# Kernel optimization log

Measured on AMD Instinct MI355X. Metric: run time of the kernel, lower is better.

The kernel has to match this reference:

```python
import jax, jax.numpy as jnp
import numpy as np

V = 32000   # vocab
T = 256     # context len
C = 384     # n_embed
H = 6       # heads
D = 64      # head dim (HEAD_SIZE // NUM_HEADS)
L = 6       # blocks
B = 16      # batch
FF = 4 * C


def setup_inputs() -> dict:
    key = jax.random.key(0)
    ks = jax.random.split(key, 16)
    s = 0.02
    p = {}
    p["x_ids"] = jax.random.randint(ks[0], (B, T), 0, V)
    p["y_ids"] = jax.random.randint(ks[1], (B, T), 0, V)
    p["tok_emb"] = jax.random.normal(ks[2], (V, C), jnp.float32) * s
    p["pos_emb"] = jax.random.normal(ks[3], (T, C), jnp.float32) * s
    p["Wq"] = jax.random.normal(ks[4], (L, H, C, D), jnp.float32) * s
    p["Wk"] = jax.random.normal(ks[5], (L, H, C, D), jnp.float32) * s
    p["Wv"] = jax.random.normal(ks[6], (L, H, C, D), jnp.float32) * s
    p["Wo"] = jax.random.normal(ks[7], (L, H * D, C), jnp.float32) * s
    p["bo"] = jnp.zeros((L, C), jnp.float32)
    p["ln1_s"] = jnp.ones((L, C), jnp.float32)
    p["ln1_b"] = jnp.zeros((L, C), jnp.float32)
    p["ln2_s"] = jnp.ones((L, C), jnp.float32)
    p["ln2_b"] = jnp.zeros((L, C), jnp.float32)
    p["W1"] = jax.random.normal(ks[8], (L, C, FF), jnp.float32) * s
    p["b1"] = jnp.zeros((L, FF), jnp.float32)
    p["W2"] = jax.random.normal(ks[9], (L, FF, C), jnp.float32) * s
    p["b2"] = jnp.zeros((L, C), jnp.float32)
    p["lnf_s"] = jnp.ones((C,), jnp.float32)
    p["lnf_b"] = jnp.zeros((C,), jnp.float32)
    p["Whead"] = jax.random.normal(ks[10], (C, V), jnp.float32) * s
    p["bhead"] = jnp.zeros((V,), jnp.float32)
    return p


def _ln(x, scale, bias, eps=1e-5):
    m = x.mean(-1, keepdims=True)
    v = ((x - m) ** 2).mean(-1, keepdims=True)
    return (x - m) * jax.lax.rsqrt(v + eps) * scale + bias


def reference(x_ids, y_ids, tok_emb, pos_emb, Wq, Wk, Wv, Wo, bo,
              ln1_s, ln1_b, ln2_s, ln2_b, W1, b1, W2, b2,
              lnf_s, lnf_b, Whead, bhead):
    Bq, Tq = x_ids.shape
    x = tok_emb[x_ids] + pos_emb[:Tq]                      # [B,T,C]
    mask = jnp.tril(jnp.ones((Tq, Tq), bool))
    scale = C ** -0.5  # NOTE: original scales by input dim C, not head dim
    for l in range(L):
        h = _ln(x, ln1_s[l], ln1_b[l])
        q = jnp.einsum('btc,hcd->bhtd', h, Wq[l])
        k = jnp.einsum('btc,hcd->bhtd', h, Wk[l])
        v = jnp.einsum('btc,hcd->bhtd', h, Wv[l])
        att = jnp.einsum('bhtd,bhsd->bhts', q, k) * scale
        att = jnp.where(mask, att, -jnp.inf)
        att = jax.nn.softmax(att, axis=-1)
        o = jnp.einsum('bhts,bhsd->bhtd', att, v)
        o = o.transpose(0, 2, 1, 3).reshape(Bq, Tq, H * D)  # concat heads
        x = x + o @ Wo[l] + bo[l]
        h2 = _ln(x, ln2_s[l], ln2_b[l])
        x = x + jax.nn.relu(h2 @ W1[l] + b1[l]) @ W2[l] + b2[l]
    x = _ln(x, lnf_s, lnf_b)
    logits = x @ Whead + bhead                             # [B,T,V]
    logp = jax.nn.log_softmax(logits, axis=-1)
    loss = -jnp.take_along_axis(logp, y_ids[..., None], axis=-1).mean()
    return (logits, loss)
```

## Files before the change

kernel.cpp:

```cpp
#include <hip/hip_runtime.h>

typedef unsigned short u16;
typedef u16   u16x4 __attribute__((ext_vector_type(4)));
typedef u16   u16x8 __attribute__((ext_vector_type(8)));
typedef short s16x8 __attribute__((ext_vector_type(8)));
typedef float f32x4 __attribute__((ext_vector_type(4)));

#define NV 32000
#define NT 256
#define NC 384
#define NH 6
#define ND 64
#define NL 6
#define NB 16
#define NFF 1536
#define NM (NB*NT)
#define QKVSZ (NB*NH*NT*ND)
#define NSLAB (NV/64)

__device__ __forceinline__ u16 f2bf(float f){
    unsigned x = __builtin_bit_cast(unsigned, f);
    x += 0x7fffu + ((x>>16)&1u);
    return (u16)(x>>16);
}

__device__ __forceinline__ void gload_lds16(const u16* g, u16* l){
    __builtin_amdgcn_global_load_lds((const __attribute__((address_space(1))) unsigned int*)g,
                                     (__attribute__((address_space(3))) unsigned int*)l, 16, 0, 0);
}

template<int N> __device__ __forceinline__ void wait_vm(){
    static_assert(N>=0 && N<=4, "add literal");
    if constexpr (N==0) asm volatile("s_waitcnt vmcnt(0)" ::: "memory");
    if constexpr (N==4) asm volatile("s_waitcnt vmcnt(4)" ::: "memory");
}
__device__ __forceinline__ void bar(){
    asm volatile("" ::: "memory");
    __builtin_amdgcn_s_barrier();
    asm volatile("" ::: "memory");
}

__global__ __launch_bounds__(256) void embed_ln(const int* __restrict__ ids,
        const float* __restrict__ tok, const float* __restrict__ pos,
        const float* __restrict__ sc, const float* __restrict__ bi,
        float* __restrict__ x, u16* __restrict__ out){
    int row  = blockIdx.x*4 + (threadIdx.x>>6);
    int lane = threadIdx.x & 63;
    int t = row & (NT-1);
    const float* tr = tok + (size_t)ids[row]*NC;
    const float* pr = pos + (size_t)t*NC;
    float* xr = x + (size_t)row*NC;
    float v[6]; float sum = 0.f, sq = 0.f;
    #pragma unroll
    for (int i=0;i<6;++i){
        int c = lane+64*i;
        v[i] = tr[c] + pr[c];
        xr[c] = v[i];
        sum += v[i]; sq += v[i]*v[i];
    }
    #pragma unroll
    for (int off=1; off<64; off<<=1){ sum += __shfl_xor(sum,off); sq += __shfl_xor(sq,off); }
    float mean = sum*(1.f/NC);
    float rstd = rsqrtf(sq*(1.f/NC) - mean*mean + 1e-5f);
    u16* orow = out + (size_t)row*NC;
    #pragma unroll
    for (int i=0;i<6;++i){ int c = lane+64*i; orow[c] = f2bf((v[i]-mean)*rstd*sc[c] + bi[c]); }
}

__global__ __launch_bounds__(256) void ln_kernel(const float* __restrict__ x,
        const float* __restrict__ sc, const float* __restrict__ bi, u16* __restrict__ out){
    int row  = blockIdx.x*4 + (threadIdx.x>>6);
    int lane = threadIdx.x & 63;
    const float* xr = x + (size_t)row*NC;
    float v[6]; float sum = 0.f, sq = 0.f;
    #pragma unroll
    for (int i=0;i<6;++i){ v[i]=xr[lane+64*i]; sum+=v[i]; sq+=v[i]*v[i]; }
    #pragma unroll
    for (int off=1; off<64; off<<=1){ sum += __shfl_xor(sum,off); sq += __shfl_xor(sq,off); }
    float mean = sum*(1.f/NC);
    float rstd = rsqrtf(sq*(1.f/NC) - mean*mean + 1e-5f);
    u16* orow = out + (size_t)row*NC;
    #pragma unroll
    for (int i=0;i<6;++i){ int c = lane+64*i; orow[c] = f2bf((v[i]-mean)*rstd*sc[c] + bi[c]); }
}

struct TDesc {
    const float* in; u16* out;
    int Cc; int nx; int perZ; int obDiv; int oStride; int start;
    long inBatch; long oS1; long oS2; float scale;
};
struct TPack { TDesc d[7]; };

__global__ __launch_bounds__(256) void tconv_all(TPack p){
    __shared__ float tile[32][33];
    int bid = blockIdx.x;
    int e = 0;
    #pragma unroll
    for (int i=1;i<7;++i) e += (bid >= p.d[i].start) ? 1 : 0;
    TDesc D = p.d[e];
    int local = bid - D.start;
    int bz  = local / D.perZ; int rem = local - bz*D.perZ;
    int cy  = rem / D.nx;     int cx  = rem - cy*D.nx;
    int r0 = cy*32, c0 = cx*32;
    const float* ib = D.in + (size_t)bz*D.inBatch;
    u16* ob = D.out + (size_t)(bz/D.obDiv)*D.oS1 + (size_t)(bz%D.obDiv)*D.oS2;
    int tx = threadIdx.x & 31, ty = threadIdx.x >> 5;
    #pragma unroll
    for (int i=0;i<4;++i) tile[ty+8*i][tx] = ib[(size_t)(r0+ty+8*i)*D.Cc + (c0+tx)];
    __syncthreads();
    #pragma unroll
    for (int i=0;i<4;++i) ob[(size_t)(c0+ty+8*i)*D.oStride + (r0+tx)] = f2bf(tile[tx][ty+8*i]*D.scale);
}

template<int EPI, int BM, int BN>
__global__ __launch_bounds__(256,4) void gemm_bt(
        const u16* __restrict__ A, const u16* __restrict__ Bt,
        const float* __restrict__ bias, float* __restrict__ resid,
        u16* __restrict__ outb,
        int M, int N, int K){
    constexpr int WM = BM/2, WN = BN/2, MI = WM/16, NI = WN/16;
    __shared__ u16 As[2*BM*32];
    __shared__ u16 Bs[2*BN*32];
    int tid = threadIdx.x;
    int lane = tid & 63, wid = tid >> 6;
    int wm = wid >> 1, wn = wid & 1;
    int l15 = lane & 15, lg = lane >> 4;
    int bx = blockIdx.x, by = blockIdx.y;
    int m0 = by * BM, n0 = bx * BN;
    f32x4 acc[MI][NI];
    #pragma unroll
    for (int a=0;a<MI;++a)
        #pragma unroll
        for (int b=0;b<NI;++b) acc[a][b] = f32x4{0.f,0.f,0.f,0.f};

    int nk = K >> 6;
    for (int kk = 0; kk < nk; ++kk){
        int k0 = kk << 6;
        #pragma unroll
        for (int h=0;h<2;++h){
            if constexpr (BM >= 64){
                #pragma unroll
                for (int i=0;i<BM/64;++i){
                    int o   = i*4096 + tid*16;
                    int row = o >> 6;
                    int kb  = (o & 63) >> 1;
                    gload_lds16(A + (size_t)(m0+row)*K + (k0+h*32+kb), &As[h*BM*32 + (o>>1)]);
                }
            } else {
                if (tid < BM*4){
                    int o = tid*16;
                    int row = o >> 6;
                    int kb  = (o & 63) >> 1;
                    gload_lds16(A + (size_t)(m0+row)*K + (k0+h*32+kb), &As[h*BM*32 + (o>>1)]);
                }
            }
            #pragma unroll
            for (int i=0;i<BN/64;++i){
                int o   = i*4096 + tid*16;
                int row = o >> 6;
                int kb  = (o & 63) >> 1;
                gload_lds16(Bt + (size_t)(n0+row)*K + (k0+h*32+kb), &Bs[h*BN*32 + (o>>1)]);
            }
        }
        asm volatile("s_waitcnt vmcnt(0)" ::: "memory");
        __syncthreads();
        #pragma unroll
        for (int ks=0;ks<2;++ks){
            s16x8 af[MI];
            #pragma unroll
            for (int mi=0;mi<MI;++mi) af[mi] = *(const s16x8*)&As[ks*BM*32 + (wm*WM+mi*16+l15)*32 + lg*8];
            #pragma unroll
            for (int ni=0;ni<NI;++ni){
                s16x8 bfr = *(const s16x8*)&Bs[ks*BN*32 + (wn*WN+ni*16+l15)*32 + lg*8];
                #pragma unroll
                for (int mi=0;mi<MI;++mi)
                    acc[mi][ni] = __builtin_amdgcn_mfma_f32_16x16x32_bf16(af[mi], bfr, acc[mi][ni], 0,0,0);
            }
        }
        __syncthreads();
    }

    #pragma unroll
    for (int mi=0;mi<MI;++mi){
        #pragma unroll
        for (int ni=0;ni<NI;++ni){
            if (EPI == 0){
                int ng = n0 + wn*WN + ni*16 + l15;
                int which = ng / NC; int hd = ng - which*NC;
                int hh = hd >> 6, d = hd & 63;
                int mgb = m0 + wm*WM + mi*16 + lg*4;
                int bb = mgb >> 8, tt = mgb & (NT-1);
                if (which == 2){
                    u16x4 v;
                    #pragma unroll
                    for (int r=0;r<4;++r) v[r] = f2bf(acc[mi][ni][r]);
                    *(u16x4*)(outb + (size_t)2*QKVSZ + ((size_t)(bb*NH+hh)*ND + d)*NT + tt) = v;
                } else {
                    #pragma unroll
                    for (int r=0;r<4;++r)
                        outb[(size_t)which*QKVSZ + ((size_t)(bb*NH+hh)*NT + tt+r)*ND + d] = f2bf(acc[mi][ni][r]);
                }
            } else {
                #pragma unroll
                for (int r=0;r<4;++r){
                    int mg = m0 + wm*WM + mi*16 + lg*4 + r;
                    int ng = n0 + wn*WN + ni*16 + l15;
                    float c = acc[mi][ni][r];
                    if (EPI == 1){
                        float* pp = resid + (size_t)mg*N + ng;
                        *pp = *pp + c + bias[ng];
                    } else if (EPI == 2){
                        outb[(size_t)mg*N + ng] = f2bf(fmaxf(c + bias[ng], 0.f));
                    }
                }
            }
        }
    }
}

__global__ __launch_bounds__(256,4) void gemm_head(
        const u16* __restrict__ A, const u16* __restrict__ Bt,
        const float* __restrict__ bias,
        float* __restrict__ outf, float* __restrict__ lpart,
        int M, int N, int K){
    constexpr int BM=128, BN=128, WM=64, WN=64, MI=4, NI=4;
    __shared__ u16 As[2][BM*32];
    __shared__ u16 Bs[2][BN*32];
    int tid = threadIdx.x;
    int lane = tid & 63, wid = tid >> 6;
    int wm = wid >> 1, wn = wid & 1;
    int l15 = lane & 15, lg = lane >> 4;
    int nwg = gridDim.x*gridDim.y;
    int orig = blockIdx.y*gridDim.x + blockIdx.x;
    int swz = (orig&7)*(nwg>>3) + (orig>>3);
    int by = swz & 31;
    int bx = swz >> 5;
    int m0 = by * BM, n0 = bx * BN;
    f32x4 acc[MI][NI];
    #pragma unroll
    for (int a=0;a<MI;++a)
        #pragma unroll
        for (int b=0;b<NI;++b) acc[a][b] = f32x4{0.f,0.f,0.f,0.f};

    auto STAGE = [&](int kt, int buf){
        int k0 = kt << 5;
        #pragma unroll
        for (int i=0;i<2;++i){
            int o   = i*4096 + tid*16;
            int row = o >> 6;
            int kb  = (o & 63) >> 1;
            gload_lds16(A + (size_t)(m0+row)*K + (k0+kb), &As[buf][o>>1]);
        }
        #pragma unroll
        for (int i=0;i<2;++i){
            int o   = i*4096 + tid*16;
            int row = o >> 6;
            int kb  = (o & 63) >> 1;
            gload_lds16(Bt + (size_t)(n0+row)*K + (k0+kb), &Bs[buf][o>>1]);
        }
    };

    int nk = K >> 5;
    STAGE(0, 0);
    for (int t = 0; t < nk; ++t){
        int buf = t & 1;
        if (t+1 < nk){ STAGE(t+1, buf^1); wait_vm<4>(); }
        else         { wait_vm<0>(); }
        bar();
        s16x8 af[MI];
        #pragma unroll
        for (int mi=0;mi<MI;++mi) af[mi] = *(const s16x8*)&As[buf][(wm*WM+mi*16+l15)*32 + lg*8];
        #pragma unroll
        for (int ni=0;ni<NI;++ni){
            s16x8 bfr = *(const s16x8*)&Bs[buf][(wn*WN+ni*16+l15)*32 + lg*8];
            #pragma unroll
            for (int mi=0;mi<MI;++mi)
                acc[mi][ni] = __builtin_amdgcn_mfma_f32_16x16x32_bf16(af[mi], bfr, acc[mi][ni], 0,0,0);
        }
        bar();
    }

    float es[MI][4];
    #pragma unroll
    for (int mi=0;mi<MI;++mi)
        #pragma unroll
        for (int r=0;r<4;++r) es[mi][r] = 0.f;
    #pragma unroll
    for (int mi=0;mi<MI;++mi)
        #pragma unroll
        for (int ni=0;ni<NI;++ni)
            #pragma unroll
            for (int r=0;r<4;++r){
                int mg = m0 + wm*WM + mi*16 + lg*4 + r;
                int ng = n0 + wn*WN + ni*16 + l15;
                float val = acc[mi][ni][r] + bias[ng];
                outf[(size_t)mg*N + ng] = val;
                es[mi][r] += __expf(val);
            }
    #pragma unroll
    for (int mi=0;mi<MI;++mi)
        #pragma unroll
        for (int r=0;r<4;++r){
            float s = es[mi][r];
            s += __shfl_xor(s,1); s += __shfl_xor(s,2);
            s += __shfl_xor(s,4); s += __shfl_xor(s,8);
            if (l15 == 0){
                int mg = m0 + wm*WM + mi*16 + lg*4 + r;
                lpart[(size_t)mg*NSLAB + bx*2 + wn] = s;
            }
        }
}

__global__ __launch_bounds__(256,2) void attn_kernel(const u16* __restrict__ qkv, u16* __restrict__ o){
    int blk = blockIdx.x;
    int qt = blk & 3, bh = blk >> 2;
    int b = bh / NH, h = bh - b*NH;
    int tid = threadIdx.x, lane = tid & 63, w = tid >> 6;
    int l15 = lane & 15, lg = lane >> 4;
    __shared__ u16 Ks[256*72];
    __shared__ u16 Vt[64*264];
    __shared__ u16 Ps[4][16*72];
    const u16* qb = qkv + (size_t)bh*NT*ND;
    const u16* kb = qkv + QKVSZ + (size_t)bh*NT*ND;
    const u16* vb = qkv + (size_t)2*QKVSZ + (size_t)bh*ND*NT;
    int nit = (qt+1)*2;
    for (int it=0; it<nit; ++it){
        int e0 = (it*256 + tid)*8;
        int row = e0 >> 6, col = e0 & 63;
        *(u16x8*)&Ks[row*72+col] = *(const u16x8*)(kb + e0);
    }
    for (int kt2=0; kt2<=qt; ++kt2){
        #pragma unroll
        for (int it=0; it<2; ++it){
            int e0 = (it*256 + tid)*8;
            int d = e0 >> 6, t = e0 & 63;
            *(u16x8*)&Vt[d*264 + kt2*64 + t] = *(const u16x8*)(vb + (size_t)d*NT + kt2*64 + t);
        }
    }
    const u16* qrow = qb + (size_t)(qt*64 + w*16 + l15)*ND;
    s16x8 qf[2];
    qf[0] = *(const s16x8*)(qrow + lg*8);
    qf[1] = *(const s16x8*)(qrow + 32 + lg*8);
    __syncthreads();

    f32x4 oacc[4]; float l_[4];
    #pragma unroll
    for (int c=0;c<4;++c){ oacc[c]=f32x4{0.f,0.f,0.f,0.f}; l_[c]=0.f; }
    u16* Pw = &Ps[w][0];

    for (int kt=0; kt<=qt; ++kt){
        f32x4 sacc[4];
        #pragma unroll
        for (int c=0;c<4;++c) sacc[c]=f32x4{0.f,0.f,0.f,0.f};
        #pragma unroll
        for (int ks=0;ks<2;++ks){
            s16x8 kf[4];
            #pragma unroll
            for (int ni=0;ni<4;++ni)
                kf[ni] = *(const s16x8*)&Ks[(kt*64+ni*16+l15)*72 + ks*32 + lg*8];
            #pragma unroll
            for (int ni=0;ni<4;++ni)
                sacc[ni] = __builtin_amdgcn_mfma_f32_16x16x32_bf16(qf[ks], kf[ni], sacc[ni], 0,0,0);
        }
        if (kt == qt){
            #pragma unroll
            for (int ni=0;ni<4;++ni)
                #pragma unroll
                for (int r=0;r<4;++r)
                    if (ni*16+l15 > w*16+lg*4+r) sacc[ni][r] = -1e30f;
        }
        #pragma unroll
        for (int r=0;r<4;++r){
            float rs = 0.f;
            #pragma unroll
            for (int ni=0;ni<4;++ni){
                float p = __expf(sacc[ni][r]);
                sacc[ni][r] = p;
                rs += p;
                Pw[(lg*4+r)*72 + ni*16 + l15] = f2bf(p);
            }
            rs += __shfl_xor(rs,1); rs += __shfl_xor(rs,2);
            rs += __shfl_xor(rs,4); rs += __shfl_xor(rs,8);
            l_[r] += rs;
        }
        #pragma unroll
        for (int ks=0;ks<2;++ks){
            s16x8 pf, vf[4];
            pf = *(const s16x8*)&Pw[l15*72 + ks*32 + lg*8];
            #pragma unroll
            for (int ni=0;ni<4;++ni)
                vf[ni] = *(const s16x8*)&Vt[(ni*16+l15)*264 + kt*64 + ks*32 + lg*8];
            #pragma unroll
            for (int ni=0;ni<4;++ni)
                oacc[ni] = __builtin_amdgcn_mfma_f32_16x16x32_bf16(pf, vf[ni], oacc[ni], 0,0,0);
        }
    }
    #pragma unroll
    for (int ni=0;ni<4;++ni)
        #pragma unroll
        for (int r=0;r<4;++r){
            int t = qt*64 + w*16 + lg*4 + r;
            int d = ni*16 + l15;
            o[((size_t)(b*NT + t))*NC + h*ND + d] = f2bf(oacc[ni][r] / l_[r]);
        }
}

__global__ __launch_bounds__(256) void loss_rows2(const float* __restrict__ lpart,
        const float* __restrict__ logits, const int* __restrict__ y, float* __restrict__ rowloss){
    int row  = blockIdx.x*4 + (threadIdx.x>>6);
    int lane = threadIdx.x & 63;
    const float* pr = lpart + (size_t)row*NSLAB;
    float s = 0.f;
    for (int i = lane; i < NSLAB; i += 64) s += pr[i];
    #pragma unroll
    for (int off=1; off<64; off<<=1) s += __shfl_xor(s, off);
    if (lane==0)
        rowloss[row] = logf(s) - logits[(size_t)row*NV + y[row]];
}

__global__ __launch_bounds__(256) void loss_final(const float* __restrict__ rowloss, float* __restrict__ out){
    int tid = threadIdx.x;
    float s = 0.f;
    for (int i = tid; i < NM; i += 256) s += rowloss[i];
    #pragma unroll
    for (int off=1; off<64; off<<=1) s += __shfl_xor(s, off);
    __shared__ float ss[4];
    if ((tid&63)==0) ss[tid>>6]=s;
    __syncthreads();
    if (tid==0) out[0] = (ss[0]+ss[1]+ss[2]+ss[3]) * (1.f/NM);
}

extern "C" void kernel_launch(void* const* d_in, const int* in_sizes, int n_in,
                              void* d_out, int out_size, void* d_ws, size_t ws_size,
                              hipStream_t stream){
    const int*   x_ids = (const int*)  d_in[0];
    const int*   y_ids = (const int*)  d_in[1];
    const float* tok   = (const float*)d_in[2];
    const float* pos   = (const float*)d_in[3];
    const float* Wq    = (const float*)d_in[4];
    const float* Wk    = (const float*)d_in[5];
    const float* Wv    = (const float*)d_in[6];
    const float* Wo    = (const float*)d_in[7];
    const float* bo    = (const float*)d_in[8];
    const float* ln1s  = (const float*)d_in[9];
    const float* ln1b  = (const float*)d_in[10];
    const float* ln2s  = (const float*)d_in[11];
    const float* ln2b  = (const float*)d_in[12];
    const float* W1    = (const float*)d_in[13];
    const float* b1    = (const float*)d_in[14];
    const float* W2    = (const float*)d_in[15];
    const float* b2    = (const float*)d_in[16];
    const float* lnfs  = (const float*)d_in[17];
    const float* lnfb  = (const float*)d_in[18];
    const float* Wh    = (const float*)d_in[19];
    const float* bh    = (const float*)d_in[20];

    float* logits = (float*)d_out;
    float* lossp  = logits + (size_t)NM*NV;

    char* ws = (char*)d_ws;
    auto alloc = [&](size_t bytes)->char*{ char* p = ws; ws += (bytes + 255) & ~(size_t)255; return p; };
    float* xf    = (float*)alloc((size_t)NM*NC*4);
    u16*   hbf   = (u16*)  alloc((size_t)NM*NC*2);
    u16*   qkvb  = (u16*)  alloc((size_t)3*QKVSZ*2);
    u16*   obf   = (u16*)  alloc((size_t)NM*NC*2);
    u16*   f1bf  = (u16*)  alloc((size_t)NM*NFF*2);
    u16*   qkvw  = (u16*)  alloc((size_t)NL*1152*NC*2);
    u16*   wot   = (u16*)  alloc((size_t)NL*NC*NC*2);
    u16*   w1t   = (u16*)  alloc((size_t)NL*NFF*NC*2);
    u16*   w2t   = (u16*)  alloc((size_t)NL*NC*NFF*2);
    u16*   wht   = (u16*)  alloc((size_t)NV*NC*2);
    float* part  = (float*)alloc((size_t)NM*4);
    float* lpart = (float*)qkvb;

    const float qscale = 0.051031036307982884f;

    TPack tp;
    tp.d[0] = {Wq, qkvw + 0*(NC*NC), ND,  2,  24, NH, NC, 0,     (long)NC*ND, (long)1152*NC, (long)ND*NC, qscale};
    tp.d[1] = {Wk, qkvw + 1*(NC*NC), ND,  2,  24, NH, NC, 864,   (long)NC*ND, (long)1152*NC, (long)ND*NC, 1.f};
    tp.d[2] = {Wv, qkvw + 2*(NC*NC), ND,  2,  24, NH, NC, 1728,  (long)NC*ND, (long)1152*NC, (long)ND*NC, 1.f};
    tp.d[3] = {Wo, wot,              NC, 12, 144, 1,  NC, 2592,  (long)NC*NC, (long)NC*NC,   0,           1.f};
    tp.d[4] = {W1, w1t,             NFF, 48, 576, 1,  NC, 3456,  (long)NC*NFF,(long)NFF*NC,  0,           1.f};
    tp.d[5] = {W2, w2t,              NC, 12, 576, 1, NFF, 6912,  (long)NFF*NC,(long)NC*NFF,  0,           1.f};
    tp.d[6] = {Wh, wht,              NV,1000,12000,1, NC, 10368, 0,           0,             0,           1.f};
    tconv_all<<<22368,256,0,stream>>>(tp);

    embed_ln<<<NM/4,256,0,stream>>>(x_ids, tok, pos, ln1s, ln1b, xf, hbf);
    for (int l = 0; l < NL; ++l){
        gemm_bt<0,64,128><<<dim3(1152/128, NM/64),256,0,stream>>>(hbf, qkvw + (size_t)l*1152*NC,
                nullptr, nullptr, qkvb, NM, 1152, NC);
        attn_kernel<<<NB*NH*4,256,0,stream>>>(qkvb, obf);
        gemm_bt<1,32,128><<<dim3(NC/128, NM/32),256,0,stream>>>(obf, wot + (size_t)l*NC*NC,
                bo + l*NC, xf, nullptr, NM, NC, NC);
        ln_kernel<<<NM/4,256,0,stream>>>(xf, ln2s + l*NC, ln2b + l*NC, hbf);
        gemm_bt<2,64,128><<<dim3(NFF/128, NM/64),256,0,stream>>>(hbf, w1t + (size_t)l*NFF*NC,
                b1 + l*NFF, nullptr, f1bf, NM, NFF, NC);
        gemm_bt<1,32,128><<<dim3(NC/128, NM/32),256,0,stream>>>(f1bf, w2t + (size_t)l*NC*NFF,
                b2 + l*NC, xf, nullptr, NM, NC, NFF);
        if (l < NL-1)
            ln_kernel<<<NM/4,256,0,stream>>>(xf, ln1s + (l+1)*NC, ln1b + (l+1)*NC, hbf);
        else
            ln_kernel<<<NM/4,256,0,stream>>>(xf, lnfs, lnfb, hbf);
    }
    gemm_head<<<dim3(NV/128, NM/128),256,0,stream>>>(hbf, wht, bh, logits, lpart, NM, NV, NC);
    loss_rows2<<<NM/4,256,0,stream>>>(lpart, logits, y_ids, part);
    loss_final<<<1,256,0,stream>>>(part, lossp);
}
```

Before: 752.2 us.

## Fold LayerNorm into GEMM weights and epilogues, removing standalone LN kernels

Each standalone LayerNorm kernel is removed. The LN scale is folded into the bf16 transposed weights, and per-column vectors u=s·W and v=b·W are precomputed. The residual GEMMs now write the raw residual in bf16 along with partial row sum and sum-of-squares. The consuming GEMMs compute mean and rstd from those stats and apply rstd*(acc - mean*u) + v in their epilogue. This drops about 12 LN launches and their activation round-trips, but it adds a weight-preprocessing kernel and carries a numerical risk from running the GEMM on un-normalized bf16 inputs and from the one-pass variance.

```diff
diff --git a/kernel.cpp b/kernel.cpp
--- a/kernel.cpp
+++ b/kernel.cpp
@@ -40,54 +40,37 @@
     asm volatile("" ::: "memory");
 }
 
-__global__ __launch_bounds__(256) void embed_ln(const int* __restrict__ ids,
+__global__ __launch_bounds__(256) void embed_stats(const int* __restrict__ ids,
         const float* __restrict__ tok, const float* __restrict__ pos,
-        const float* __restrict__ sc, const float* __restrict__ bi,
-        float* __restrict__ x, u16* __restrict__ out){
+        float* __restrict__ x, u16* __restrict__ xb, float* __restrict__ statp){
     int row  = blockIdx.x*4 + (threadIdx.x>>6);
     int lane = threadIdx.x & 63;
     int t = row & (NT-1);
     const float* tr = tok + (size_t)ids[row]*NC;
     const float* pr = pos + (size_t)t*NC;
     float* xr = x + (size_t)row*NC;
-    float v[6]; float sum = 0.f, sq = 0.f;
+    u16* br = xb + (size_t)row*NC;
+    float sum = 0.f, sq = 0.f;
     #pragma unroll
     for (int i=0;i<6;++i){
         int c = lane+64*i;
-        v[i] = tr[c] + pr[c];
-        xr[c] = v[i];
-        sum += v[i]; sq += v[i]*v[i];
+        float v = tr[c] + pr[c];
+        xr[c] = v; br[c] = f2bf(v);
+        sum += v; sq += v*v;
     }
     #pragma unroll
     for (int off=1; off<64; off<<=1){ sum += __shfl_xor(sum,off); sq += __shfl_xor(sq,off); }
-    float mean = sum*(1.f/NC);
-    float rstd = rsqrtf(sq*(1.f/NC) - mean*mean + 1e-5f);
-    u16* orow = out + (size_t)row*NC;
-    #pragma unroll
-    for (int i=0;i<6;++i){ int c = lane+64*i; orow[c] = f2bf((v[i]-mean)*rstd*sc[c] + bi[c]); }
-}
-
-__global__ __launch_bounds__(256) void ln_kernel(const float* __restrict__ x,
-        const float* __restrict__ sc, const float* __restrict__ bi, u16* __restrict__ out){
-    int row  = blockIdx.x*4 + (threadIdx.x>>6);
-    int lane = threadIdx.x & 63;
-    const float* xr = x + (size_t)row*NC;
-    float v[6]; float sum = 0.f, sq = 0.f;
-    #pragma unroll
-    for (int i=0;i<6;++i){ v[i]=xr[lane+64*i]; sum+=v[i]; sq+=v[i]*v[i]; }
-    #pragma unroll
-    for (int off=1; off<64; off<<=1){ sum += __shfl_xor(sum,off); sq += __shfl_xor(sq,off); }
-    float mean = sum*(1.f/NC);
-    float rstd = rsqrtf(sq*(1.f/NC) - mean*mean + 1e-5f);
-    u16* orow = out + (size_t)row*NC;
-    #pragma unroll
-    for (int i=0;i<6;++i){ int c = lane+64*i; orow[c] = f2bf((v[i]-mean)*rstd*sc[c] + bi[c]); }
+    if (lane == 0){
+        float* pp = statp + (size_t)row*6;
+        pp[0]=sum; pp[1]=sq; pp[2]=0.f; pp[3]=0.f; pp[4]=0.f; pp[5]=0.f;
+    }
 }
 
 struct TDesc {
     const float* in; u16* out;
     int Cc; int nx; int perZ; int obDiv; int oStride; int start;
     long inBatch; long oS1; long oS2; float scale;
+    const float* svec; long svecS;
 };
 struct TPack { TDesc d[7]; };
 
@@ -104,29 +87,81 @@
     int r0 = cy*32, c0 = cx*32;
     const float* ib = D.in + (size_t)bz*D.inBatch;
     u16* ob = D.out + (size_t)(bz/D.obDiv)*D.oS1 + (size_t)(bz%D.obDiv)*D.oS2;
+    const float* sv = D.svec ? D.svec + (size_t)(bz/D.obDiv)*D.svecS : nullptr;
     int tx = threadIdx.x & 31, ty = threadIdx.x >> 5;
     #pragma unroll
     for (int i=0;i<4;++i) tile[ty+8*i][tx] = ib[(size_t)(r0+ty+8*i)*D.Cc + (c0+tx)];
     __syncthreads();
-    #pragma unroll
-    for (int i=0;i<4;++i) ob[(size_t)(c0+ty+8*i)*D.oStride + (r0+tx)] = f2bf(tile[tx][ty+8*i]*D.scale);
-}
-
-template<int EPI, int BM, int BN>
+    float f = D.scale * (sv ? sv[r0+tx] : 1.f);
+    #pragma unroll
+    for (int i=0;i<4;++i) ob[(size_t)(c0+ty+8*i)*D.oStride + (r0+tx)] = f2bf(tile[tx][ty+8*i]*f);
+}
+
+struct UVArgs {
+    const float *Wq,*Wk,*Wv,*W1,*Wh;
+    const float *ln1s,*ln1b,*ln2s,*ln2b,*lnfs,*lnfb;
+    float *uvq, *uvf, *uvh; float qscale;
+};
+__global__ __launch_bounds__(256) void uv_kernel(UVArgs a){
+    int gid = blockIdx.x*256 + threadIdx.x;
+    const float *W, *s, *b; int kst; float sc = 1.f; float *ou, *ov;
+    if (gid < 6*1152){
+        int l = gid/1152, n = gid - l*1152;
+        int which = n/384, hd = n - which*384, h = hd>>6, d = hd&63;
+        const float* Ws = which==0 ? a.Wq : (which==1 ? a.Wk : a.Wv);
+        W = Ws + ((size_t)(l*NH+h))*NC*ND + d;
+        kst = ND;
+        s = a.ln1s + l*NC; b = a.ln1b + l*NC;
+        if (which==0) sc = a.qscale;
+        ou = a.uvq + (size_t)l*2*1152 + n; ov = ou + 1152;
+    } else if (gid < 6*1152 + 6*1536){
+        int g = gid - 6*1152; int l = g/1536, f = g - l*1536;
+        W = a.W1 + (size_t)l*NC*NFF + f; kst = NFF;
+        s = a.ln2s + l*NC; b = a.ln2b + l*NC;
+        ou = a.uvf + (size_t)l*2*1536 + f; ov = ou + 1536;
+    } else {
+        int n = gid - (6*1152 + 6*1536);
+        W = a.Wh + n; kst = NV;
+        s = a.lnfs; b = a.lnfb;
+        ou = a.uvh + n; ov = ou + NV;
+    }
+    float u = 0.f, v = 0.f;
+    for (int k=0;k<NC;++k){ float w = W[(size_t)k*kst]; u += s[k]*w; v += b[k]*w; }
+    *ou = u*sc; *ov = v*sc;
+}
+
+template<int EPI, int BM, int BN, int LNF>
 __global__ __launch_bounds__(256,4) void gemm_bt(
         const u16* __restrict__ A, const u16* __restrict__ Bt,
         const float* __restrict__ bias, float* __restrict__ resid,
         u16* __restrict__ outb,
+        const float* __restrict__ statp, const float* __restrict__ uvec,
+        const float* __restrict__ vvec, float* __restrict__ stout,
         int M, int N, int K){
     constexpr int WM = BM/2, WN = BN/2, MI = WM/16, NI = WN/16;
     __shared__ u16 As[2*BM*32];
     __shared__ u16 Bs[2*BN*32];
+    __shared__ float stM[LNF?BM:1], stR[LNF?BM:1];
+    __shared__ float sS[2][16][2], sQ[2][16][2];
     int tid = threadIdx.x;
     int lane = tid & 63, wid = tid >> 6;
     int wm = wid >> 1, wn = wid & 1;
     int l15 = lane & 15, lg = lane >> 4;
     int bx = blockIdx.x, by = blockIdx.y;
     int m0 = by * BM, n0 = bx * BN;
+
+    if constexpr (LNF){
+        if (tid < BM){
+            const float* pp = statp + (size_t)(m0+tid)*6;
+            float s = pp[0]+pp[2]+pp[4];
+            float q = pp[1]+pp[3]+pp[5];
+            float mu = s*(1.f/NC);
+            stM[tid] = mu;
+            stR[tid] = rsqrtf(q*(1.f/NC) - mu*mu + 1e-5f);
+        }
+        __syncthreads();
+    }
+
     f32x4 acc[MI][NI];
     #pragma unroll
     for (int a=0;a<MI;++a)
@@ -180,38 +215,74 @@
         __syncthreads();
     }
 
+    if (EPI == 1){
+        float rs[4]={0.f,0.f,0.f,0.f}, rq[4]={0.f,0.f,0.f,0.f};
+        #pragma unroll
+        for (int ni=0;ni<NI;++ni)
+            #pragma unroll
+            for (int r=0;r<4;++r){
+                int mg = m0 + wm*WM + lg*4 + r;
+                int ng = n0 + wn*WN + ni*16 + l15;
+                float* pp = resid + (size_t)mg*NC + ng;
+                float val = acc[0][ni][r] + bias[ng] + *pp;
+                *pp = val;
+                outb[(size_t)mg*NC + ng] = f2bf(val);
+                rs[r] += val; rq[r] += val*val;
+            }
+        #pragma unroll
+        for (int r=0;r<4;++r){
+            rs[r]+=__shfl_xor(rs[r],1); rq[r]+=__shfl_xor(rq[r],1);
+            rs[r]+=__shfl_xor(rs[r],2); rq[r]+=__shfl_xor(rq[r],2);
+            rs[r]+=__shfl_xor(rs[r],4); rq[r]+=__shfl_xor(rq[r],4);
+            rs[r]+=__shfl_xor(rs[r],8); rq[r]+=__shfl_xor(rq[r],8);
+            if (l15==0){ sS[wm][lg*4+r][wn]=rs[r]; sQ[wm][lg*4+r][wn]=rq[r]; }
+        }
+        __syncthreads();
+        if (tid < 32){
+            int wmi = tid>>4, rr = tid&15;
+            float s = sS[wmi][rr][0] + sS[wmi][rr][1];
+            float q = sQ[wmi][rr][0] + sQ[wmi][rr][1];
+            float* pp = stout + (size_t)(m0+tid)*6 + bx*2;
+            pp[0]=s; pp[1]=q;
+        }
+        return;
+    }
+
     #pragma unroll
     for (int mi=0;mi<MI;++mi){
         #pragma unroll
         for (int ni=0;ni<NI;++ni){
+            int ng = n0 + wn*WN + ni*16 + l15;
             if (EPI == 0){
-                int ng = n0 + wn*WN + ni*16 + l15;
                 int which = ng / NC; int hd = ng - which*NC;
                 int hh = hd >> 6, d = hd & 63;
                 int mgb = m0 + wm*WM + mi*16 + lg*4;
                 int bb = mgb >> 8, tt = mgb & (NT-1);
+                float uu = uvec[ng], vv0 = vvec[ng];
                 if (which == 2){
                     u16x4 v;
                     #pragma unroll
-                    for (int r=0;r<4;++r) v[r] = f2bf(acc[mi][ni][r]);
+                    for (int r=0;r<4;++r){
+                        int lr = wm*WM + mi*16 + lg*4 + r;
+                        v[r] = f2bf(stR[lr]*(acc[mi][ni][r] - stM[lr]*uu) + vv0);
+                    }
                     *(u16x4*)(outb + (size_t)2*QKVSZ + ((size_t)(bb*NH+hh)*ND + d)*NT + tt) = v;
                 } else {
                     #pragma unroll
-                    for (int r=0;r<4;++r)
-                        outb[(size_t)which*QKVSZ + ((size_t)(bb*NH+hh)*NT + tt+r)*ND + d] = f2bf(acc[mi][ni][r]);
+                    for (int r=0;r<4;++r){
+                        int lr = wm*WM + mi*16 + lg*4 + r;
+                        float val = stR[lr]*(acc[mi][ni][r] - stM[lr]*uu) + vv0;
+                        outb[(size_t)which*QKVSZ + ((size_t)(bb*NH+hh)*NT + tt+r)*ND + d] = f2bf(val);
+                    }
                 }
             } else {
+                float uu = uvec[ng], vv0 = vvec[ng] + bias[ng];
                 #pragma unroll
                 for (int r=0;r<4;++r){
-                    int mg = m0 + wm*WM + mi*16 + lg*4 + r;
-                    int ng = n0 + wn*WN + ni*16 + l15;
-                    float c = acc[mi][ni][r];
-                    if (EPI == 1){
-                        float* pp = resid + (size_t)mg*N + ng;
-                        *pp = *pp + c + bias[ng];
-                    } else if (EPI == 2){
-                        outb[(size_t)mg*N + ng] = f2bf(fmaxf(c + bias[ng], 0.f));
-                    }
+                    int lr = wm*WM + mi*16 + lg*4 + r;
+                    int mg = m0 + lr;
+                    float val = stR[lr]*(acc[mi][ni][r] - stM[lr]*uu) + vv0;
+                    outb[(size_t)mg*N + ng] = f2bf(fmaxf(val, 0.f));
                 }
             }
         }
@@ -221,11 +292,14 @@
 __global__ __launch_bounds__(256,4) void gemm_head(
         const u16* __restrict__ A, const u16* __restrict__ Bt,
         const float* __restrict__ bias,
+        const float* __restrict__ statp, const float* __restrict__ uvec,
+        const float* __restrict__ vvec,
         float* __restrict__ outf, float* __restrict__ lpart,
         int M, int N, int K){
     constexpr int BM=128, BN=128, WM=64, WN=64, MI=4, NI=4;
     __shared__ u16 As[2][BM*32];
     __shared__ u16 Bs[2][BN*32];
+    __shared__ float stM[BM], stR[BM];
     int tid = threadIdx.x;
     int lane = tid & 63, wid = tid >> 6;
     int wm = wid >> 1, wn = wid & 1;
@@ -236,6 +310,17 @@
     int by = swz & 31;
     int bx = swz >> 5;
     int m0 = by * BM, n0 = bx * BN;
+
+    if (tid < BM){
+        const float* pp = statp + (size_t)(m0+tid)*6;
+        float s = pp[0]+pp[2]+pp[4];
+        float q = pp[1]+pp[3]+pp[5];
+        float mu = s*(1.f/NC);
+        stM[tid] = mu;
+        stR[tid] = rsqrtf(q*(1.f/NC) - mu*mu + 1e-5f);
+    }
+    __syncthreads();
+
     f32x4 acc[MI][NI];
     #pragma unroll
     for (int a=0;a<MI;++a)
@@ -288,15 +373,18 @@
     #pragma unroll
     for (int mi=0;mi<MI;++mi)
         #pragma unroll
-        for (int ni=0;ni<NI;++ni)
+        for (int ni=0;ni<NI;++ni){
+            int ng = n0 + wn*WN + ni*16 + l15;
+            float uu = uvec[ng], vv0 = vvec[ng] + bias[ng];
             #pragma unroll
             for (int r=0;r<4;++r){
-                int mg = m0 + wm*WM + mi*16 + lg*4 + r;
-                int ng = n0 + wn*WN + ni*16 + l15;
-                float val = acc[mi][ni][r] + bias[ng];
+                int lr = wm*WM + mi*16 + lg*4 + r;
+                int mg = m0 + lr;
+                float val = stR[lr]*(acc[mi][ni][r] - stM[lr]*uu) + vv0;
                 outf[(size_t)mg*N + ng] = val;
                 es[mi][r] += __expf(val);
             }
+        }
     #pragma unroll
     for (int mi=0;mi<MI;++mi)
         #pragma unroll
@@ -461,7 +549,8 @@
     char* ws = (char*)d_ws;
     auto alloc = [&](size_t bytes)->char*{ char* p = ws; ws += (bytes + 255) & ~(size_t)255; return p; };
     float* xf    = (float*)alloc((size_t)NM*NC*4);
-    u16*   hbf   = (u16*)  alloc((size_t)NM*NC*2);
+    u16*   xb    = (u16*)  alloc((size_t)NM*NC*2);
+    float* statp = (float*)alloc((size_t)NM*6*4);
     u16*   qkvb  = (u16*)  alloc((size_t)3*QKVSZ*2);
     u16*   obf   = (u16*)  alloc((size_t)NM*NC*2);
     u16*   f1bf  = (u16*)  alloc((size_t)NM*NFF*2);
@@ -470,39 +559,47 @@
     u16*   w1t   = (u16*)  alloc((size_t)NL*NFF*NC*2);
     u16*   w2t   = (u16*)  alloc((size_t)NL*NC*NFF*2);
     u16*   wht   = (u16*)  alloc((size_t)NV*NC*2);
+    float* uvq   = (float*)alloc((size_t)NL*2*1152*4);
+    float* uvf   = (float*)alloc((size_t)NL*2*1536*4);
+    float* uvh   = (float*)alloc((size_t)2*NV*4);
     float* part  = (float*)alloc((size_t)NM*4);
     float* lpart = (float*)qkvb;
 
     const float qscale = 0.051031036307982884f;
 
     TPack tp;
-    tp.d[0] = {Wq, qkvw + 0*(NC*NC), ND,  2,  24, NH, NC, 0,     (long)NC*ND, (long)1152*NC, (long)ND*NC, qscale};
-    tp.d[1] = {Wk, qkvw + 1*(NC*NC), ND,  2,  24, NH, NC, 864,   (long)NC*ND, (long)1152*NC, (long)ND*NC, 1.f};
-    tp.d[2] = {Wv, qkvw + 2*(NC*NC), ND,  2,  24, NH, NC, 1728,  (long)NC*ND, (long)1152*NC, (long)ND*NC, 1.f};
-    tp.d[3] = {Wo, wot,              NC, 12, 144, 1,  NC, 2592,  (long)NC*NC, (long)NC*NC,   0,           1.f};
-    tp.d[4] = {W1, w1t,             NFF, 48, 576, 1,  NC, 3456,  (long)NC*NFF,(long)NFF*NC,  0,           1.f};
-    tp.d[5] = {W2, w2t,              NC, 12, 576, 1, NFF, 6912,  (long)NFF*NC,(long)NC*NFF,  0,           1.f};
-    tp.d[6] = {Wh, wht,              NV,1000,12000,1, NC, 10368, 0,           0,             0,           1.f};
+    tp.d[0] = {Wq, qkvw + 0*(NC*NC), ND,  2,  24, NH, NC, 0,     (long)NC*ND, (long)1152*NC, (long)ND*NC, qscale, ln1s, NC};
+    tp.d[1] = {Wk, qkvw + 1*(NC*NC), ND,  2,  24, NH, NC, 864,   (long)NC*ND, (long)1152*NC, (long)ND*NC, 1.f,    ln1s, NC};
+    tp.d[2] = {Wv, qkvw + 2*(NC*NC), ND,  2,  24, NH, NC, 1728,  (long)NC*ND, (long)1152*NC, (long)ND*NC, 1.f,    ln1s, NC};
+    tp.d[3] = {Wo, wot,              NC, 12, 144, 1,  NC, 2592,  (long)NC*NC, (long)NC*NC,   0,           1.f,    nullptr, 0};
+    tp.d[4] = {W1, w1t,             NFF, 48, 576, 1,  NC, 3456,  (long)NC*NFF,(long)NFF*NC,  0,           1.f,    ln2s, NC};
+    tp.d[5] = {W2, w2t,              NC, 12, 576, 1, NFF, 6912,  (long)NFF*NC,(long)NC*NFF,  0,           1.f,    nullptr, 0};
+    tp.d[6] = {Wh, wht,              NV,1000,12000,1, NC, 10368, 0,           0,             0,           1.f,    lnfs, 0};
     tconv_all<<<22368,256,0,stream>>>(tp);
 
-    embed_ln<<<NM/4,256,0,stream>>>(x_ids, tok, pos, ln1s, ln1b, xf, hbf);
+    UVArgs ua = {Wq, Wk, Wv, W1, Wh, ln1s, ln1b, ln2s, ln2b, lnfs, lnfb, uvq, uvf, uvh, qscale};
+    uv_kernel<<<(6*1152 + 6*1536 + NV)/256, 256, 0, stream>>>(ua);
+
+    embed_stats<<<NM/4,256,0,stream>>>(x_ids, tok, pos, xf, xb, statp);
     for (int l = 0; l < NL; ++l){
-        gemm_bt<0,64,128><<<dim3(1152/128, NM/64),256,0,stream>>>(hbf, qkvw + (size_t)l*1152*NC,
-                nullptr, nullptr, qkvb, NM, 1152, NC);
+        gemm_bt<0,64,128,1><<<dim3(1152/128, NM/64),256,0,stream>>>(
+                xb, qkvw + (size_t)l*1152*NC, nullptr, nullptr, qkvb,
+                statp, uvq + (size_t)l*2*1152, uvq + (size_t)l*2*1152 + 1152, nullptr,
+                NM, 1152, NC);
         attn_kernel<<<NB*NH*4,256,0,stream>>>(qkvb, obf);
-        gemm_bt<1,32,128><<<dim3(NC/128, NM/32),256,0,stream>>>(obf, wot + (size_t)l*NC*NC,
-                bo + l*NC, xf, nullptr, NM, NC, NC);
-        ln_kernel<<<NM/4,256,0,stream>>>(xf, ln2s + l*NC, ln2b + l*NC, hbf);
-        gemm_bt<2,64,128><<<dim3(NFF/128, NM/64),256,0,stream>>>(hbf, w1t + (size_t)l*NFF*NC,
-                b1 + l*NFF, nullptr, f1bf, NM, NFF, NC);
-        gemm_bt<1,32,128><<<dim3(NC/128, NM/32),256,0,stream>>>(f1bf, w2t + (size_t)l*NC*NFF,
-                b2 + l*NC, xf, nullptr, NM, NC, NFF);
-        if (l < NL-1)
-            ln_kernel<<<NM/4,256,0,stream>>>(xf, ln1s + (l+1)*NC, ln1b + (l+1)*NC, hbf);
-        else
-            ln_kernel<<<NM/4,256,0,stream>>>(xf, lnfs, lnfb, hbf);
-    }
-    gemm_head<<<dim3(NV/128, NM/128),256,0,stream>>>(hbf, wht, bh, logits, lpart, NM, NV, NC);
+        gemm_bt<1,32,128,0><<<dim3(NC/128, NM/32),256,0,stream>>>(
+                obf, wot + (size_t)l*NC*NC, bo + l*NC, xf, xb,
+                nullptr, nullptr, nullptr, statp, NM, NC, NC);
+        gemm_bt<2,64,128,1><<<dim3(NFF/128, NM/64),256,0,stream>>>(
+                xb, w1t + (size_t)l*NFF*NC, b1 + l*NFF, nullptr, f1bf,
+                statp, uvf + (size_t)l*2*1536, uvf + (size_t)l*2*1536 + 1536, nullptr,
+                NM, NFF, NC);
+        gemm_bt<1,32,128,0><<<dim3(NC/128, NM/32),256,0,stream>>>(
+                f1bf, w2t + (size_t)l*NC*NFF, b2 + l*NC, xf, xb,
+                nullptr, nullptr, nullptr, statp, NM, NC, NFF);
+    }
+    gemm_head<<<dim3(NV/128, NM/128),256,0,stream>>>(xb, wht, bh,
+            statp, uvh, uvh + NV, logits, lpart, NM, NV, NC);
     loss_rows2<<<NM/4,256,0,stream>>>(lpart, logits, y_ids, part);
     loss_final<<<1,256,0,stream>>>(part, lossp);
 }
```

Result: no change. 750.3 us (-0.3%).
